# Kernel tuning notes

Hardware: AMD Instinct MI355X
Metric: run time of the kernel (lower is better)

## Reference

```python
import jax, jax.numpy as jnp
import numpy as np

EPS = 1e-5


def _gcn_conv(x, src, dst, norm, W, b, n_nodes):
    # PyG GCNConv: transform, then normalized scatter-add aggregation (self-loops included in src/dst)
    h = x @ W                                   # [N, out]
    msg = h[src] * norm[:, None]                # gather over edges [E+N, out]
    agg = jax.ops.segment_sum(msg, dst, num_segments=n_nodes)
    return agg + b


def _bn(x, gamma, beta):
    # BatchNorm1d in training mode: batch stats over node axis, biased variance
    mu = jnp.mean(x, axis=0)
    var = jnp.mean((x - mu) ** 2, axis=0)
    return (x - mu) * jax.lax.rsqrt(var + EPS) * gamma + beta


def setup_inputs() -> dict:
    key = jax.random.key(0)
    ks = jax.random.split(key, 8)
    N, E, F_in, H, F_out = 50000, 800000, 32, 96, 2
    x = jax.random.normal(ks[0], (N, F_in), dtype=jnp.float32)
    edge_index = jax.random.randint(ks[1], (2, E), 0, N, dtype=jnp.int64)
    def lin(k, fi, fo):
        s = 1.0 / np.sqrt(fi)
        return jax.random.uniform(k, (fi, fo), jnp.float32, -s, s)
    W1 = lin(ks[2], F_in, H); b1 = jnp.zeros((H,), jnp.float32)
    W2 = lin(ks[3], H, H);    b2 = jnp.zeros((H,), jnp.float32)
    W3 = lin(ks[4], H, H);    b3 = jnp.zeros((H,), jnp.float32)
    W4 = lin(ks[5], H, F_out); b4 = jnp.zeros((F_out,), jnp.float32)
    g1 = jnp.ones((H,), jnp.float32); be1 = jnp.zeros((H,), jnp.float32)
    g2 = jnp.ones((H,), jnp.float32); be2 = jnp.zeros((H,), jnp.float32)
    g3 = jnp.ones((H,), jnp.float32); be3 = jnp.zeros((H,), jnp.float32)
    return dict(x=x, edge_index=edge_index,
                W1=W1, b1=b1, g1=g1, be1=be1,
                W2=W2, b2=b2, g2=g2, be2=be2,
                W3=W3, b3=b3, g3=g3, be3=be3,
                W4=W4, b4=b4)


def reference(x, edge_index, W1, b1, g1, be1, W2, b2, g2, be2, W3, b3, g3, be3, W4, b4):
    N = x.shape[0]
    loop = jnp.arange(N, dtype=edge_index.dtype)
    src = jnp.concatenate([edge_index[0], loop])   # add self-loops
    dst = jnp.concatenate([edge_index[1], loop])
    deg = jax.ops.segment_sum(jnp.ones_like(dst, dtype=x.dtype), dst, num_segments=N)
    dinv = jnp.where(deg > 0, jax.lax.rsqrt(deg), 0.0)
    norm = dinv[src] * dinv[dst]                   # D^{-1/2} (A+I) D^{-1/2}

    h = jax.nn.relu(_bn(_gcn_conv(x, src, dst, norm, W1, b1, N), g1, be1))
    h = jax.nn.relu(_bn(_gcn_conv(h, src, dst, norm, W2, b2, N), g2, be2))
    h = jax.nn.relu(_bn(_gcn_conv(h, src, dst, norm, W3, b3, N), g3, be3))
    return _gcn_conv(h, src, dst, norm, W4, b4, N)
```

## Files before the change

### kernel.cpp

```cpp
#include <hip/hip_runtime.h>
#include <hip/hip_bf16.h>

using bf16x8 = __attribute__((ext_vector_type(8))) short;
using f32x4  = __attribute__((ext_vector_type(4))) float;

#define FS_CHUNK 4096

__device__ __forceinline__ float ldf(const void* p, size_t i, float isf){
  if (isf > 0.5f) return ((const float*)p)[i];
  unsigned int u = ((unsigned int)((const unsigned short*)p)[i]) << 16;
  return __uint_as_float(u);
}
__device__ __forceinline__ unsigned short f2bf(float v){
  unsigned int u = __float_as_uint(v);
  u = (u + 0x7FFFu + ((u >> 16) & 1u)) >> 16;
  return (unsigned short)u;
}
__device__ __forceinline__ unsigned int pk2(float a, float b){
  return (unsigned int)f2bf(a) | ((unsigned int)f2bf(b) << 16);
}
__device__ __forceinline__ float lo16(unsigned int u){ return __uint_as_float(u << 16); }
__device__ __forceinline__ float hi16(unsigned int u){ return __uint_as_float(u & 0xFFFF0000u); }

__global__ void k_fill(unsigned short* o, unsigned short v, int n){
  int i = blockIdx.x*blockDim.x + threadIdx.x;
  if (i < n) o[i] = v;
}

__global__ void k_prep(const unsigned short* xh, const unsigned int* eu,
                       float* flag, int nelemX, long long E,
                       const void* W1, const void* W2, const void* W3, const void* W4,
                       unsigned short* __restrict__ Wt1, unsigned short* __restrict__ Wt2,
                       unsigned short* __restrict__ Wt3, float* __restrict__ W4f,
                       int* __restrict__ cnt, float* __restrict__ stAll, int n){
  int t = threadIdx.x;
  if (blockIdx.x > 0){
    int total = n + 4609;
    for (int i = (int)(blockIdx.x-1)*256 + t; i < total; i += (int)(gridDim.x-1)*256){
      if (i < n) cnt[i] = 0; else stAll[i - n] = 0.f;
    }
    return;
  }
  __shared__ int sf32, si64;
  __shared__ float sisf;
  if (t == 0){ sf32 = 0; si64 = 1; }
  __syncthreads();
  {
    int i = 2*t;
    if (i < nelemX){
      unsigned e8 = (xh[i] >> 7) & 0xFFu;
      if (e8 >= 140u) sf32 = 1;
    }
    if ((long long)(2*t + 1) < 2*E){
      if (eu[2*t + 1] != 0u) si64 = 0;
    }
  }
  __syncthreads();
  if (t == 0){
    flag[0] = (float)sf32; flag[1] = (float)si64;
    sisf = (float)sf32;
  }
  __syncthreads();
  float isf = sisf;
  for (int q = t; q < 3072; q += 256){
    int nn = q >> 5, k = q & 31;
    Wt1[q] = f2bf(ldf(W1, (size_t)96*k + nn, isf));
  }
  for (int q = t; q < 9216; q += 256){
    int nn = q/96, k = q - 96*nn;
    Wt2[q] = f2bf(ldf(W2, (size_t)96*k + nn, isf));
    Wt3[q] = f2bf(ldf(W3, (size_t)96*k + nn, isf));
  }
  if (t < 192) W4f[t] = ldf(W4, t, isf);
}

__global__ void k_cnt2(const int* __restrict__ ei, const float* __restrict__ flag,
                       int* __restrict__ cnt, int* __restrict__ ec,
                       long long E, int n){
  long long i = (long long)blockIdx.x*blockDim.x + threadIdx.x;
  long long i0 = 2*i;
  if (i0 >= E) return;
  bool i64 = (flag[1] > 0.5f);
  bool two = (i0 + 1 < E);
  int s0, d0, s1 = 0, d1 = -1;
  if ((E & 1LL) == 0){
    if (i64){
      uint4 vs = ((const uint4*)ei)[i];
      uint4 vd = ((const uint4*)(ei + 2*E))[i];
      s0 = (int)vs.x; s1 = (int)vs.z; d0 = (int)vd.x; d1 = (int)vd.z;
    } else {
      int2 vs = ((const int2*)ei)[i];
      int2 vd = ((const int2*)(ei + E))[i];
      s0 = vs.x; s1 = vs.y; d0 = vd.x; d1 = vd.y;
    }
  } else {
    if (i64){ s0 = ei[2*i0]; d0 = ei[2*E + 2*i0];
              if (two){ s1 = ei[2*i0+2]; d1 = ei[2*E + 2*i0 + 2]; } }
    else    { s0 = ei[i0];   d0 = ei[E + i0];
              if (two){ s1 = ei[i0+1];   d1 = ei[E + i0 + 1]; } }
  }
  bool ok0 = ((unsigned)s0 < (unsigned)n) && ((unsigned)d0 < (unsigned)n);
  bool ok1 = two && ((unsigned)s1 < (unsigned)n) && ((unsigned)d1 < (unsigned)n);
  if (!ok0){ s0 = -1; d0 = -1; }
  if (!ok1){ s1 = -1; d1 = -1; }
  if (two){
    int4 o; o.x = s0; o.y = d0; o.z = s1; o.w = d1;
    ((int4*)ec)[i] = o;
  } else {
    int2 o; o.x = s0; o.y = d0;
    ((int2*)ec)[i0] = o;
  }
  if (ok0) atomicAdd(&cnt[d0], 1);
  if (ok1) atomicAdd(&cnt[d1], 1);
}

__global__ void k_emit2(const int* __restrict__ cnt, int* __restrict__ gctr,
                        int* __restrict__ rowst, int* __restrict__ cursor,
                        float* __restrict__ dinv, int n){
  int i = blockIdx.x*256 + threadIdx.x;
  int lane = threadIdx.x & 63;
  int v = (i < n) ? cnt[i] : 0;
  int s = v;
  #pragma unroll
  for (int off = 1; off < 64; off <<= 1){
    int u = __shfl_up(s, off, 64);
    if (lane >= off) s += u;
  }
  int wtot = __shfl(s, 63, 64);
  int base = 0;
  if (lane == 63) base = atomicAdd(gctr, wtot);
  base = __shfl(base, 63, 64);
  if (i < n){
    int r = base + s - v;
    rowst[i]  = r;
    cursor[i] = r;
    dinv[i]   = rsqrtf((float)(1 + v));
  }
}

template<typename IT>
__global__ __launch_bounds__(256) void k_fx(const int* __restrict__ ec,
      int* __restrict__ cursor, IT* __restrict__ csr,
      long long E, int n, int gF8,
      const void* __restrict__ x, const float* __restrict__ flag,
      const float* __restrict__ dinv, unsigned short* __restrict__ XS){
  int t = threadIdx.x;
  if ((int)blockIdx.x < gF8){
    int part = blockIdx.x & 7;
    long long base = (long long)(blockIdx.x >> 3) * FS_CHUNK;
    int pl = (int)(((long long)n *  part     ) >> 3);
    int pr = (int)(((long long)n * (part + 1)) >> 3);
    long long lim = base + FS_CHUNK < E ? base + FS_CHUNK : E;
    for (long long i = base + 2*t; i < lim; i += 512){
      int4 v = ((const int4*)ec)[i >> 1];
      if (v.y >= pl && v.y < pr && (unsigned)v.x < (unsigned)n){
        int p = atomicAdd(&cursor[v.y], 1);
        csr[p] = (IT)v.x;
      }
      if (i + 1 < lim && v.w >= pl && v.w < pr && (unsigned)v.z < (unsigned)n){
        int p = atomicAdd(&cursor[v.w], 1);
        csr[p] = (IT)v.z;
      }
    }
    return;
  }
  int q = (int)(blockIdx.x - gF8)*256 + t;
  if (q < 4*n){
    int node = q >> 2, part = q & 3;
    float isf = flag[0];
    float di = dinv[node];
    uint4 o;
    if (isf > 0.5f){
      const float* xr = (const float*)x + (size_t)32*node + 8*part;
      o.x = pk2(xr[0]*di, xr[1]*di); o.y = pk2(xr[2]*di, xr[3]*di);
      o.z = pk2(xr[4]*di, xr[5]*di); o.w = pk2(xr[6]*di, xr[7]*di);
    } else {
      uint4 v = ((const uint4*)x)[(size_t)4*node + part];
      o.x = pk2(lo16(v.x)*di, hi16(v.x)*di);
      o.y = pk2(lo16(v.y)*di, hi16(v.y)*di);
      o.z = pk2(lo16(v.z)*di, hi16(v.z)*di);
      o.w = pk2(lo16(v.w)*di, hi16(v.w)*di);
    }
    ((uint4*)XS)[q] = o;
  }
}

#define ACC8(v) { a0+=lo16((v).x); a1+=hi16((v).x); a2+=lo16((v).y); a3+=hi16((v).y); \
                  a4+=lo16((v).z); a5+=hi16((v).z); a6+=lo16((v).w); a7+=hi16((v).w); }

template<typename IT>
__global__ __launch_bounds__(256) void k_aggx(const uint4* __restrict__ xs4,
      const int* __restrict__ rowst, const int* __restrict__ cnt,
      const IT* __restrict__ csr, const float* __restrict__ dinv,
      const unsigned short* __restrict__ Wt1b,
      unsigned short* __restrict__ Zb, float* __restrict__ stout, int n){
  __shared__ __align__(16) unsigned short Xs[64][40];
  __shared__ __align__(16) unsigned short Wt[96][40];
  __shared__ float bs[96], bq[96];
  int t = threadIdx.x;
  for (int q = t; q < 384; q += 256){
    uint4 v = ((const uint4*)Wt1b)[q];
    *(uint4*)&Wt[q >> 2][(q & 3)*8] = v;
  }
  if (t < 96){ bs[t] = 0.f; bq[t] = 0.f; }
  int g = t & 3, ty = t >> 2;
  int node = blockIdx.x*64 + ty;
  float a0=0.f,a1=0.f,a2=0.f,a3=0.f,a4=0.f,a5=0.f,a6=0.f,a7=0.f;
  if (node < n){
    uint4 v = xs4[(size_t)node*4 + g];
    ACC8(v);
    int b = rowst[node], e = b + cnt[node];
    int j = b;
    for (; j + 7 < e; j += 8){
      uint4 v0 = xs4[(size_t)csr[j]  *4 + g];
      uint4 v1 = xs4[(size_t)csr[j+1]*4 + g];
      uint4 v2 = xs4[(size_t)csr[j+2]*4 + g];
      uint4 v3 = xs4[(size_t)csr[j+3]*4 + g];
      uint4 v4 = xs4[(size_t)csr[j+4]*4 + g];
      uint4 v5 = xs4[(size_t)csr[j+5]*4 + g];
      uint4 v6 = xs4[(size_t)csr[j+6]*4 + g];
      uint4 v7 = xs4[(size_t)csr[j+7]*4 + g];
      ACC8(v0); ACC8(v1); ACC8(v2); ACC8(v3);
      ACC8(v4); ACC8(v5); ACC8(v6); ACC8(v7);
    }
    for (; j + 3 < e; j += 4){
      uint4 v0 = xs4[(size_t)csr[j]  *4 + g];
      uint4 v1 = xs4[(size_t)csr[j+1]*4 + g];
      uint4 v2 = xs4[(size_t)csr[j+2]*4 + g];
      uint4 v3 = xs4[(size_t)csr[j+3]*4 + g];
      ACC8(v0); ACC8(v1); ACC8(v2); ACC8(v3);
    }
    for (; j < e; ++j){
      uint4 vv = xs4[(size_t)csr[j]*4 + g];
      ACC8(vv);
    }
    float di = dinv[node];
    a0*=di; a1*=di; a2*=di; a3*=di; a4*=di; a5*=di; a6*=di; a7*=di;
  }
  uint4 o;
  o.x = pk2(a0,a1); o.y = pk2(a2,a3); o.z = pk2(a4,a5); o.w = pk2(a6,a7);
  *(uint4*)&Xs[ty][8*g] = o;
  __syncthreads();
  int wv = t >> 6, lane = t & 63;
  int m = lane & 15, quad = lane >> 4;
  bf16x8 av = *(const bf16x8*)&Xs[16*wv + m][8*quad];
  f32x4 acc[6];
  #pragma unroll
  for (int c = 0; c < 6; ++c) acc[c] = (f32x4)(0.f);
  #pragma unroll
  for (int c = 0; c < 6; ++c){
    bf16x8 bv = *(const bf16x8*)&Wt[16*c + m][8*quad];
    acc[c] = __builtin_amdgcn_mfma_f32_16x16x32_bf16(av, bv, acc[c], 0, 0, 0);
  }
  int rowbase = blockIdx.x*64 + 16*wv + 4*quad;
  #pragma unroll
  for (int c = 0; c < 6; ++c){
    int col = 16*c + m;
    float s = 0.f, q = 0.f;
    #pragma unroll
    for (int r = 0; r < 4; ++r){
      int rr = rowbase + r;
      if (rr < n){
        unsigned short h = f2bf(acc[c][r]);
        Zb[(size_t)96*rr + col] = h;
        float br = __uint_as_float(((unsigned int)h) << 16);
        s += br; q += br*br;
      }
    }
    atomicAdd(&bs[col], s);
    atomicAdd(&bq[col], q);
  }
  __syncthreads();
  if (t < 96){
    int rep = blockIdx.x & 7;
    atomicAdd(&stout[192*rep + t],      bs[t]);
    atomicAdd(&stout[192*rep + 96 + t], bq[t]);
  }
}

template<typename IT>
__global__ __launch_bounds__(192) void k_agg(const uint4* __restrict__ hsr,
      const int* __restrict__ rowst, const int* __restrict__ cnt,
      const IT* __restrict__ csr,
      const float* __restrict__ dinv, uint4* __restrict__ zb4,
      float* __restrict__ stout, int n){
  __shared__ float ls[16][97], lq[16][97];
  int g = threadIdx.x, ty = threadIdx.y;
  int t = ty*12 + g;
  int node = blockIdx.x*16 + ty;
  float r[8];
  if (node < n){
    uint4 v = hsr[(size_t)node*12 + g];
    float a0 = lo16(v.x), a1 = hi16(v.x), a2 = lo16(v.y), a3 = hi16(v.y);
    float a4 = lo16(v.z), a5 = hi16(v.z), a6 = lo16(v.w), a7 = hi16(v.w);
    int b = rowst[node], e = b + cnt[node];
    int j = b;
    for (; j + 7 < e; j += 8){
      uint4 v0 = hsr[(size_t)csr[j]  *12 + g];
      uint4 v1 = hsr[(size_t)csr[j+1]*12 + g];
      uint4 v2 = hsr[(size_t)csr[j+2]*12 + g];
      uint4 v3 = hsr[(size_t)csr[j+3]*12 + g];
      uint4 v4 = hsr[(size_t)csr[j+4]*12 + g];
      uint4 v5 = hsr[(size_t)csr[j+5]*12 + g];
      uint4 v6 = hsr[(size_t)csr[j+6]*12 + g];
      uint4 v7 = hsr[(size_t)csr[j+7]*12 + g];
      ACC8(v0); ACC8(v1); ACC8(v2); ACC8(v3);
      ACC8(v4); ACC8(v5); ACC8(v6); ACC8(v7);
    }
    for (; j + 3 < e; j += 4){
      uint4 v0 = hsr[(size_t)csr[j]  *12 + g];
      uint4 v1 = hsr[(size_t)csr[j+1]*12 + g];
      uint4 v2 = hsr[(size_t)csr[j+2]*12 + g];
      uint4 v3 = hsr[(size_t)csr[j+3]*12 + g];
      ACC8(v0); ACC8(v1); ACC8(v2); ACC8(v3);
    }
    for (; j < e; ++j){
      uint4 vv = hsr[(size_t)csr[j]*12 + g];
      ACC8(vv);
    }
    float di = dinv[node];
    uint4 o;
    o.x = pk2(a0*di, a1*di);
    o.y = pk2(a2*di, a3*di);
    o.z = pk2(a4*di, a5*di);
    o.w = pk2(a6*di, a7*di);
    zb4[(size_t)node*12 + g] = o;
    r[0]=lo16(o.x); r[1]=hi16(o.x); r[2]=lo16(o.y); r[3]=hi16(o.y);
    r[4]=lo16(o.z); r[5]=hi16(o.z); r[6]=lo16(o.w); r[7]=hi16(o.w);
  } else {
    #pragma unroll
    for (int jj = 0; jj < 8; ++jj) r[jj] = 0.f;
  }
  #pragma unroll
  for (int jj = 0; jj < 8; ++jj){
    ls[ty][8*g + jj] = r[jj];
    lq[ty][8*g + jj] = r[jj]*r[jj];
  }
  __syncthreads();
  if (t < 96){
    float s = 0.f, q = 0.f;
    #pragma unroll
    for (int rr = 0; rr < 16; ++rr){ s += ls[rr][t]; q += lq[rr][t]; }
    int rep = blockIdx.x & 7;
    atomicAdd(&stout[192*rep + t],      s);
    atomicAdd(&stout[192*rep + 96 + t], q);
  }
}

__global__ __launch_bounds__(256) void k_linm(const unsigned short* __restrict__ zb,
      const unsigned short* __restrict__ Wtb, const float* __restrict__ st,
      const void* __restrict__ gam, const void* __restrict__ bet,
      const float* __restrict__ flag, const float* __restrict__ dinv,
      unsigned short* __restrict__ HS, int n, float invN){
  __shared__ float sa[96], sc[96];
  __shared__ __align__(16) unsigned short Ys[64][104];
  __shared__ __align__(16) unsigned short Wt[96][104];
  int t = threadIdx.x;
  if (t < 96){
    float ssum = 0.f, qsum = 0.f;
    #pragma unroll
    for (int r = 0; r < 8; ++r){ ssum += st[192*r + t]; qsum += st[192*r + 96 + t]; }
    float isf = flag[0];
    float mu  = ssum*invN;
    float var = fmaxf(qsum*invN - mu*mu, 0.f);
    float istd = rsqrtf(var + 1e-5f);
    float a = ldf(gam, t, isf)*istd;
    sa[t] = a; sc[t] = ldf(bet, t, isf) - mu*a;
  }
  for (int q = t; q < 1152; q += 256){
    uint4 v = ((const uint4*)Wtb)[q];
    *(uint4*)&Wt[q/12][8*(q - 12*(q/12))] = v;
  }
  __syncthreads();
  {
    int row = t >> 2, part = t & 3;
    int node = blockIdx.x*64 + row;
    if (node < n){
      const uint4* zr = (const uint4*)(zb + (size_t)96*node) + 3*part;
      #pragma unroll
      for (int q = 0; q < 3; ++q){
        uint4 zz = zr[q];
        int k = 24*part + 8*q;
        float y0 = fmaxf(lo16(zz.x)*sa[k]   + sc[k],   0.f);
        float y1 = fmaxf(hi16(zz.x)*sa[k+1] + sc[k+1], 0.f);
        float y2 = fmaxf(lo16(zz.y)*sa[k+2] + sc[k+2], 0.f);
        float y3 = fmaxf(hi16(zz.y)*sa[k+3] + sc[k+3], 0.f);
        float y4 = fmaxf(lo16(zz.z)*sa[k+4] + sc[k+4], 0.f);
        float y5 = fmaxf(hi16(zz.z)*sa[k+5] + sc[k+5], 0.f);
        float y6 = fmaxf(lo16(zz.w)*sa[k+6] + sc[k+6], 0.f);
        float y7 = fmaxf(hi16(zz.w)*sa[k+7] + sc[k+7], 0.f);
        *(unsigned int*)&Ys[row][k]     = pk2(y0, y1);
        *(unsigned int*)&Ys[row][k + 2] = pk2(y2, y3);
        *(unsigned int*)&Ys[row][k + 4] = pk2(y4, y5);
        *(unsigned int*)&Ys[row][k + 6] = pk2(y6, y7);
      }
    } else {
      unsigned int* yp = (unsigned int*)&Ys[row][24*part];
      #pragma unroll
      for (int q = 0; q < 12; ++q) yp[q] = 0u;
    }
  }
  __syncthreads();
  int wv = t >> 6, lane = t & 63;
  int m = lane & 15, quad = lane >> 4;
  bf16x8 av[3];
  #pragma unroll
  for (int kt = 0; kt < 3; ++kt)
    av[kt] = *(const bf16x8*)&Ys[16*wv + m][32*kt + 8*quad];
  f32x4 acc[6];
  #pragma unroll
  for (int c = 0; c < 6; ++c) acc[c] = (f32x4)(0.f);
  #pragma unroll
  for (int c = 0; c < 6; ++c){
    const unsigned short* wrow = &Wt[16*c + m][8*quad];
    #pragma unroll
    for (int kt = 0; kt < 3; ++kt){
      bf16x8 bv = *(const bf16x8*)(wrow + 32*kt);
      acc[c] = __builtin_amdgcn_mfma_f32_16x16x32_bf16(av[kt], bv, acc[c], 0, 0, 0);
    }
  }
  int rowbase = blockIdx.x*64 + 16*wv + 4*quad;
  float div[4];
  #pragma unroll
  for (int r = 0; r < 4; ++r){ int rr = rowbase + r; div[r] = (rr < n) ? dinv[rr] : 0.f; }
  #pragma unroll
  for (int c = 0; c < 6; ++c){
    int col = 16*c + m;
    #pragma unroll
    for (int r = 0; r < 4; ++r){
      int rr = rowbase + r;
      if (rr < n) HS[(size_t)96*rr + col] = f2bf(acc[c][r]*div[r]);
    }
  }
}

__global__ __launch_bounds__(256) void k_lin4(const unsigned short* __restrict__ zb,
      const float* __restrict__ Wf, const float* __restrict__ st,
      const void* __restrict__ gam, const void* __restrict__ bet,
      const float* __restrict__ flag, const float* __restrict__ dinv,
      float* __restrict__ hs2, int n, float invN){
  __shared__ float sa[96], sc[96];
  int t = threadIdx.x;
  if (t < 96){
    float ssum = 0.f, qsum = 0.f;
    #pragma unroll
    for (int r = 0; r < 8; ++r){ ssum += st[192*r + t]; qsum += st[192*r + 96 + t]; }
    float isf = flag[0];
    float mu  = ssum*invN;
    float var = fmaxf(qsum*invN - mu*mu, 0.f);
    float istd = rsqrtf(var + 1e-5f);
    float a = ldf(gam, t, isf)*istd;
    sa[t] = a; sc[t] = ldf(bet, t, isf) - mu*a;
  }
  __syncthreads();
  int i = blockIdx.x*blockDim.x + t;
  if (i >= n) return;
  const uint4* zr = (const uint4*)(zb + (size_t)96*i);
  float a0 = 0.f, a1 = 0.f;
  #pragma unroll
  for (int q = 0; q < 12; ++q){
    uint4 zz = zr[q];
    int k = 8*q;
    float y;
    y = fmaxf(lo16(zz.x)*sa[k]   + sc[k],   0.f); a0 += y*Wf[2*k];    a1 += y*Wf[2*k+1];
    y = fmaxf(hi16(zz.x)*sa[k+1] + sc[k+1], 0.f); a0 += y*Wf[2*k+2];  a1 += y*Wf[2*k+3];
    y = fmaxf(lo16(zz.y)*sa[k+2] + sc[k+2], 0.f); a0 += y*Wf[2*k+4];  a1 += y*Wf[2*k+5];
    y = fmaxf(hi16(zz.y)*sa[k+3] + sc[k+3], 0.f); a0 += y*Wf[2*k+6];  a1 += y*Wf[2*k+7];
    y = fmaxf(lo16(zz.z)*sa[k+4] + sc[k+4], 0.f); a0 += y*Wf[2*k+8];  a1 += y*Wf[2*k+9];
    y = fmaxf(hi16(zz.z)*sa[k+5] + sc[k+5], 0.f); a0 += y*Wf[2*k+10]; a1 += y*Wf[2*k+11];
    y = fmaxf(lo16(zz.w)*sa[k+6] + sc[k+6], 0.f); a0 += y*Wf[2*k+12]; a1 += y*Wf[2*k+13];
    y = fmaxf(hi16(zz.w)*sa[k+7] + sc[k+7], 0.f); a0 += y*Wf[2*k+14]; a1 += y*Wf[2*k+15];
  }
  float di = dinv[i];
  hs2[(size_t)2*i]   = di*a0;
  hs2[(size_t)2*i+1] = di*a1;
}

template<typename IT>
__global__ void k_agg2(const float2* __restrict__ hs2, const int* __restrict__ rowst,
                       const int* __restrict__ cnt, const IT* __restrict__ csr,
                       const float* __restrict__ dinv,
                       const void* __restrict__ b4, const float* __restrict__ flag,
                       void* __restrict__ out, int n){
  int node = blockIdx.x*blockDim.x + threadIdx.x;
  if (node >= n) return;
  float2 a = hs2[node];
  int b = rowst[node], e = b + cnt[node];
  int j = b;
  for (; j + 3 < e; j += 4){
    float2 v0 = hs2[(size_t)csr[j]];
    float2 v1 = hs2[(size_t)csr[j+1]];
    float2 v2 = hs2[(size_t)csr[j+2]];
    float2 v3 = hs2[(size_t)csr[j+3]];
    a.x += v0.x + v1.x + v2.x + v3.x;
    a.y += v0.y + v1.y + v2.y + v3.y;
  }
  for (; j < e; ++j){
    float2 v = hs2[(size_t)csr[j]];
    a.x += v.x; a.y += v.y;
  }
  float isf = flag[0];
  float di = dinv[node];
  float v0 = a.x*di + ldf(b4, 0, isf);
  float v1 = a.y*di + ldf(b4, 1, isf);
  if (isf > 0.5f){
    ((float*)out)[(size_t)2*node]   = v0;
    ((float*)out)[(size_t)2*node+1] = v1;
  } else {
    ((unsigned short*)out)[(size_t)2*node]   = f2bf(v0);
    ((unsigned short*)out)[(size_t)2*node+1] = f2bf(v1);
  }
}

extern "C" void kernel_launch(void* const* d_in, const int* in_sizes, int n_in,
                              void* d_out, int out_size, void* d_ws, size_t ws_size,
                              hipStream_t stream)
{
  const int B = 256;
  unsigned short* outh = (unsigned short*)d_out;

  if (n_in < 16){
    k_fill<<<(out_size+B-1)/B, B, 0, stream>>>(outh, 0x3F40u, out_size); return;
  }
  const int N = in_sizes[0] / 32;
  const long long E = in_sizes[1] / 2;
  if (in_sizes[0] % 32 != 0 || out_size != 2*N){
    k_fill<<<(out_size+B-1)/B, B, 0, stream>>>(outh, 0x3F60u, out_size); return;
  }
  const bool u16 = (N < 65536);

  size_t Npad = ((size_t)N + 3) & ~(size_t)3;
  float* ws   = (float*)d_ws;
  float* dinv = ws;
  float* hs2  = dinv + Npad;
  float* flag = hs2 + (size_t)2*N;
  float* stAll= flag + 4;
  float* W4f  = stAll + 4612;
  unsigned short* Wt1b = (unsigned short*)(W4f + 192);
  unsigned short* Wt2b = Wt1b + 3072;
  unsigned short* Wt3b = Wt2b + 9216;
  int* cnt    = (int*)(Wt3b + 9216);
  int* cursor = cnt + N;
  int* rowst  = cursor + N;
  void* csrv  = (void*)(rowst + N);
  size_t csrBytes = (size_t)E * (u16 ? 2 : 4);
  uintptr_t hp_ = (uintptr_t)csrv + csrBytes;
  hp_ = (hp_ + 15) & ~(uintptr_t)15;
  unsigned short* HS = (unsigned short*)hp_;
  unsigned short* Zb = HS + (size_t)96*N;
  int* ec = (int*)(Zb + (size_t)96*N);

  size_t needB = ((uintptr_t)(ec + 2*E + 4) - (uintptr_t)d_ws) + 64;
  if (ws_size < needB){
    k_fill<<<(out_size+B-1)/B, B, 0, stream>>>(outh, 0x3F00u, out_size); return;
  }

  unsigned short* XS = HS;

  const void* x  = d_in[0];
  const int*  ei = (const int*)d_in[1];
  const void* W1 = d_in[2];
  const void* g1 = d_in[4];  const void* be1 = d_in[5];
  const void* W2 = d_in[6];
  const void* g2 = d_in[8];  const void* be2 = d_in[9];
  const void* W3 = d_in[10];
  const void* g3 = d_in[12]; const void* be3 = d_in[13];
  const void* W4 = d_in[14];
  const void* b4 = d_in[15];

  float* stA = stAll;
  float* stB = stAll + 1536;
  float* stC = stAll + 3072;
  int*   gctr = (int*)(stAll + 4608);

  int gN  = (N + B - 1)/B;
  long long hE = (E + 1)/2;
  int gE2 = (int)((hE + B - 1)/B); if (gE2 < 1) gE2 = 1;
  int nb  = (N + 255)/256;
  int gA  = (N + 15)/16;
  int gL  = (N + 63)/64;
  int gXS = (4*N + 255)/256;
  int gF8 = (int)((E + FS_CHUNK - 1)/FS_CHUNK) * 8;
  float invN = 1.0f / (float)N;
  dim3 ablk(12,16);

  k_prep<<<33, B, 0, stream>>>((const unsigned short*)x, (const unsigned int*)ei,
                               flag, in_sizes[0], E, W1, W2, W3, W4,
                               Wt1b, Wt2b, Wt3b, W4f, cnt, stAll, N);
  k_cnt2<<<gE2, B, 0, stream>>>(ei, flag, cnt, ec, E, N);
  k_emit2<<<nb, B, 0, stream>>>(cnt, gctr, rowst, cursor, dinv, N);

  if (u16){
    unsigned short* csr = (unsigned short*)csrv;
    k_fx<unsigned short><<<gF8 + gXS, B, 0, stream>>>(ec, cursor, csr, E, N, gF8,
                                                      x, flag, dinv, XS);
    k_aggx<unsigned short><<<gL, B, 0, stream>>>((const uint4*)XS, rowst, cnt, csr, dinv, Wt1b, Zb, stA, N);
    k_linm<<<gL, B, 0, stream>>>(Zb, Wt2b, stA, g1, be1, flag, dinv, HS, N, invN);
    k_agg<unsigned short><<<gA, ablk, 0, stream>>>((const uint4*)HS, rowst, cnt, csr, dinv, (uint4*)Zb, stB, N);
    k_linm<<<gL, B, 0, stream>>>(Zb, Wt3b, stB, g2, be2, flag, dinv, HS, N, invN);
    k_agg<unsigned short><<<gA, ablk, 0, stream>>>((const uint4*)HS, rowst, cnt, csr, dinv, (uint4*)Zb, stC, N);
    k_lin4<<<gN, B, 0, stream>>>(Zb, W4f, stC, g3, be3, flag, dinv, hs2, N, invN);
    k_agg2<unsigned short><<<gN, B, 0, stream>>>((const float2*)hs2, rowst, cnt, csr, dinv, b4, flag, d_out, N);
  } else {
    int* csr = (int*)csrv;
    k_fx<int><<<gF8 + gXS, B, 0, stream>>>(ec, cursor, csr, E, N, gF8,
                                           x, flag, dinv, XS);
    k_aggx<int><<<gL, B, 0, stream>>>((const uint4*)XS, rowst, cnt, csr, dinv, Wt1b, Zb, stA, N);
    k_linm<<<gL, B, 0, stream>>>(Zb, Wt2b, stA, g1, be1, flag, dinv, HS, N, invN);
    k_agg<int><<<gA, ablk, 0, stream>>>((const uint4*)HS, rowst, cnt, csr, dinv, (uint4*)Zb, stB, N);
    k_linm<<<gL, B, 0, stream>>>(Zb, Wt3b, stB, g2, be2, flag, dinv, HS, N, invN);
    k_agg<int><<<gA, ablk, 0, stream>>>((const uint4*)HS, rowst, cnt, csr, dinv, (uint4*)Zb, stC, N);
    k_lin4<<<gN, B, 0, stream>>>(Zb, W4f, stC, g3, be3, flag, dinv, hs2, N, invN);
    k_agg2<int><<<gN, B, 0, stream>>>((const float2*)hs2, rowst, cnt, csr, dinv, b4, flag, d_out, N);
  }
}
```

Baseline: 329.9 us.

## Fuse BN-ReLU-linear into aggregation by reordering aggregate-then-transform

Replaces the separate k_linm and k_agg kernels for layers 2 and 3 with one k_aggf kernel. It applies the previous layer's BatchNorm affine and ReLU on the fly to gathered neighbour rows, aggregates them, then multiplies by the weight with MFMA and accumulates the BN statistics. This uses linearity to aggregate before transforming. It also stores a per-edge dinv[src] array alongside the CSR so the gather does not need a second indirect lookup. Two launches per layer become one and an intermediate round trip through global memory is dropped. The cost is redoing the affine and ReLU for every edge, an extra 4 bytes read per edge, and more per-block weight loading because blocks shrink to 16 nodes.

New measurement: 349.9 us. 6.1% more time.

```diff
diff --git a/kernel.cpp b/kernel.cpp
--- a/kernel.cpp
+++ b/kernel.cpp
@@ -140,7 +140,7 @@
 
 template<typename IT>
 __global__ __launch_bounds__(256) void k_fx(const int* __restrict__ ec,
-      int* __restrict__ cursor, IT* __restrict__ csr,
+      int* __restrict__ cursor, IT* __restrict__ csr, float* __restrict__ csrd,
       long long E, int n, int gF8,
       const void* __restrict__ x, const float* __restrict__ flag,
       const float* __restrict__ dinv, unsigned short* __restrict__ XS){
@@ -156,10 +156,12 @@
       if (v.y >= pl && v.y < pr && (unsigned)v.x < (unsigned)n){
         int p = atomicAdd(&cursor[v.y], 1);
         csr[p] = (IT)v.x;
+        csrd[p] = dinv[v.x];
       }
       if (i + 1 < lim && v.w >= pl && v.w < pr && (unsigned)v.z < (unsigned)n){
         int p = atomicAdd(&cursor[v.w], 1);
         csr[p] = (IT)v.z;
+        csrd[p] = dinv[v.z];
       }
     }
     return;
@@ -278,88 +280,35 @@
   }
 }
 
+#define AFF8(v,d) { float y_; \
+  y_ = fmaxf(fmaf(lo16((v).x), A0, C0), 0.f); a0 = fmaf(y_, (d), a0); \
+  y_ = fmaxf(fmaf(hi16((v).x), A1, C1), 0.f); a1 = fmaf(y_, (d), a1); \
+  y_ = fmaxf(fmaf(lo16((v).y), A2, C2), 0.f); a2 = fmaf(y_, (d), a2); \
+  y_ = fmaxf(fmaf(hi16((v).y), A3, C3), 0.f); a3 = fmaf(y_, (d), a3); \
+  y_ = fmaxf(fmaf(lo16((v).z), A4, C4), 0.f); a4 = fmaf(y_, (d), a4); \
+  y_ = fmaxf(fmaf(hi16((v).z), A5, C5), 0.f); a5 = fmaf(y_, (d), a5); \
+  y_ = fmaxf(fmaf(lo16((v).w), A6, C6), 0.f); a6 = fmaf(y_, (d), a6); \
+  y_ = fmaxf(fmaf(hi16((v).w), A7, C7), 0.f); a7 = fmaf(y_, (d), a7); }
+
 template<typename IT>
-__global__ __launch_bounds__(192) void k_agg(const uint4* __restrict__ hsr,
+__global__ __launch_bounds__(192) void k_aggf(const uint4* __restrict__ zsrc,
       const int* __restrict__ rowst, const int* __restrict__ cnt,
-      const IT* __restrict__ csr,
-      const float* __restrict__ dinv, uint4* __restrict__ zb4,
-      float* __restrict__ stout, int n){
-  __shared__ float ls[16][97], lq[16][97];
-  int g = threadIdx.x, ty = threadIdx.y;
-  int t = ty*12 + g;
-  int node = blockIdx.x*16 + ty;
-  float r[8];
-  if (node < n){
-    uint4 v = hsr[(size_t)node*12 + g];
-    float a0 = lo16(v.x), a1 = hi16(v.x), a2 = lo16(v.y), a3 = hi16(v.y);
-    float a4 = lo16(v.z), a5 = hi16(v.z), a6 = lo16(v.w), a7 = hi16(v.w);
-    int b = rowst[node], e = b + cnt[node];
-    int j = b;
-    for (; j + 7 < e; j += 8){
-      uint4 v0 = hsr[(size_t)csr[j]  *12 + g];
-      uint4 v1 = hsr[(size_t)csr[j+1]*12 + g];
-      uint4 v2 = hsr[(size_t)csr[j+2]*12 + g];
-      uint4 v3 = hsr[(size_t)csr[j+3]*12 + g];
-      uint4 v4 = hsr[(size_t)csr[j+4]*12 + g];
-      uint4 v5 = hsr[(size_t)csr[j+5]*12 + g];
-      uint4 v6 = hsr[(size_t)csr[j+6]*12 + g];
-      uint4 v7 = hsr[(size_t)csr[j+7]*12 + g];
-      ACC8(v0); ACC8(v1); ACC8(v2); ACC8(v3);
-      ACC8(v4); ACC8(v5); ACC8(v6); ACC8(v7);
-    }
-    for (; j + 3 < e; j += 4){
-      uint4 v0 = hsr[(size_t)csr[j]  *12 + g];
-      uint4 v1 = hsr[(size_t)csr[j+1]*12 + g];
-      uint4 v2 = hsr[(size_t)csr[j+2]*12 + g];
-      uint4 v3 = hsr[(size_t)csr[j+3]*12 + g];
-      ACC8(v0); ACC8(v1); ACC8(v2); ACC8(v3);
-    }
-    for (; j < e; ++j){
-      uint4 vv = hsr[(size_t)csr[j]*12 + g];
-      ACC8(vv);
-    }
-    float di = dinv[node];
-    uint4 o;
-    o.x = pk2(a0*di, a1*di);
-    o.y = pk2(a2*di, a3*di);
-    o.z = pk2(a4*di, a5*di);
-    o.w = pk2(a6*di, a7*di);
-    zb4[(size_t)node*12 + g] = o;
-    r[0]=lo16(o.x); r[1]=hi16(o.x); r[2]=lo16(o.y); r[3]=hi16(o.y);
-    r[4]=lo16(o.z); r[5]=hi16(o.z); r[6]=lo16(o.w); r[7]=hi16(o.w);
-  } else {
-    #pragma unroll
-    for (int jj = 0; jj < 8; ++jj) r[jj] = 0.f;
-  }
-  #pragma unroll
-  for (int jj = 0; jj < 8; ++jj){
-    ls[ty][8*g + jj] = r[jj];
-    lq[ty][8*g + jj] = r[jj]*r[jj];
-  }
-  __syncthreads();
-  if (t < 96){
-    float s = 0.f, q = 0.f;
-    #pragma unroll
-    for (int rr = 0; rr < 16; ++rr){ s += ls[rr][t]; q += lq[rr][t]; }
-    int rep = blockIdx.x & 7;
-    atomicAdd(&stout[192*rep + t],      s);
-    atomicAdd(&stout[192*rep + 96 + t], q);
-  }
-}
-
-__global__ __launch_bounds__(256) void k_linm(const unsigned short* __restrict__ zb,
-      const unsigned short* __restrict__ Wtb, const float* __restrict__ st,
+      const IT* __restrict__ csr, const float* __restrict__ csrd,
+      const float* __restrict__ dinv,
+      const unsigned short* __restrict__ Wtb,
+      const float* __restrict__ stin,
       const void* __restrict__ gam, const void* __restrict__ bet,
-      const float* __restrict__ flag, const float* __restrict__ dinv,
-      unsigned short* __restrict__ HS, int n, float invN){
+      const float* __restrict__ flag,
+      unsigned short* __restrict__ zout, float* __restrict__ stout,
+      int n, float invN){
   __shared__ float sa[96], sc[96];
-  __shared__ __align__(16) unsigned short Ys[64][104];
+  __shared__ __align__(16) unsigned short Y[16][104];
   __shared__ __align__(16) unsigned short Wt[96][104];
   int t = threadIdx.x;
   if (t < 96){
     float ssum = 0.f, qsum = 0.f;
     #pragma unroll
-    for (int r = 0; r < 8; ++r){ ssum += st[192*r + t]; qsum += st[192*r + 96 + t]; }
+    for (int r = 0; r < 8; ++r){ ssum += stin[192*r + t]; qsum += stin[192*r + 96 + t]; }
     float isf = flag[0];
     float mu  = ssum*invN;
     float var = fmaxf(qsum*invN - mu*mu, 0.f);
@@ -367,69 +316,95 @@
     float a = ldf(gam, t, isf)*istd;
     sa[t] = a; sc[t] = ldf(bet, t, isf) - mu*a;
   }
-  for (int q = t; q < 1152; q += 256){
+  for (int q = t; q < 1152; q += 192){
     uint4 v = ((const uint4*)Wtb)[q];
-    *(uint4*)&Wt[q/12][8*(q - 12*(q/12))] = v;
-  }
-  __syncthreads();
-  {
-    int row = t >> 2, part = t & 3;
-    int node = blockIdx.x*64 + row;
-    if (node < n){
-      const uint4* zr = (const uint4*)(zb + (size_t)96*node) + 3*part;
-      #pragma unroll
-      for (int q = 0; q < 3; ++q){
-        uint4 zz = zr[q];
-        int k = 24*part + 8*q;
-        float y0 = fmaxf(lo16(zz.x)*sa[k]   + sc[k],   0.f);
-        float y1 = fmaxf(hi16(zz.x)*sa[k+1] + sc[k+1], 0.f);
-        float y2 = fmaxf(lo16(zz.y)*sa[k+2] + sc[k+2], 0.f);
-        float y3 = fmaxf(hi16(zz.y)*sa[k+3] + sc[k+3], 0.f);
-        float y4 = fmaxf(lo16(zz.z)*sa[k+4] + sc[k+4], 0.f);
-        float y5 = fmaxf(hi16(zz.z)*sa[k+5] + sc[k+5], 0.f);
-        float y6 = fmaxf(lo16(zz.w)*sa[k+6] + sc[k+6], 0.f);
-        float y7 = fmaxf(hi16(zz.w)*sa[k+7] + sc[k+7], 0.f);
-        *(unsigned int*)&Ys[row][k]     = pk2(y0, y1);
-        *(unsigned int*)&Ys[row][k + 2] = pk2(y2, y3);
-        *(unsigned int*)&Ys[row][k + 4] = pk2(y4, y5);
-        *(unsigned int*)&Ys[row][k + 6] = pk2(y6, y7);
-      }
-    } else {
-      unsigned int* yp = (unsigned int*)&Ys[row][24*part];
-      #pragma unroll
-      for (int q = 0; q < 12; ++q) yp[q] = 0u;
-    }
-  }
+    int rr = q/12;
+    *(uint4*)&Wt[rr][8*(q - 12*rr)] = v;
+  }
+  __syncthreads();
+  int g = t % 12, ty = t / 12;
+  float A0=sa[8*g],A1=sa[8*g+1],A2=sa[8*g+2],A3=sa[8*g+3],
+        A4=sa[8*g+4],A5=sa[8*g+5],A6=sa[8*g+6],A7=sa[8*g+7];
+  float C0=sc[8*g],C1=sc[8*g+1],C2=sc[8*g+2],C3=sc[8*g+3],
+        C4=sc[8*g+4],C5=sc[8*g+5],C6=sc[8*g+6],C7=sc[8*g+7];
+  int node = blockIdx.x*16 + ty;
+  float a0=0.f,a1=0.f,a2=0.f,a3=0.f,a4=0.f,a5=0.f,a6=0.f,a7=0.f;
+  if (node < n){
+    float di = dinv[node];
+    {
+      uint4 v = zsrc[(size_t)node*12 + g];
+      AFF8(v, di);
+    }
+    int b = rowst[node], e = b + cnt[node];
+    int j = b;
+    for (; j + 7 < e; j += 8){
+      uint4 v0 = zsrc[(size_t)csr[j]  *12 + g]; float d0 = csrd[j];
+      uint4 v1 = zsrc[(size_t)csr[j+1]*12 + g]; float d1 = csrd[j+1];
+      uint4 v2 = zsrc[(size_t)csr[j+2]*12 + g]; float d2 = csrd[j+2];
+      uint4 v3 = zsrc[(size_t)csr[j+3]*12 + g]; float d3 = csrd[j+3];
+      uint4 v4 = zsrc[(size_t)csr[j+4]*12 + g]; float d4 = csrd[j+4];
+      uint4 v5 = zsrc[(size_t)csr[j+5]*12 + g]; float d5 = csrd[j+5];
+      uint4 v6 = zsrc[(size_t)csr[j+6]*12 + g]; float d6 = csrd[j+6];
+      uint4 v7 = zsrc[(size_t)csr[j+7]*12 + g]; float d7 = csrd[j+7];
+      AFF8(v0,d0); AFF8(v1,d1); AFF8(v2,d2); AFF8(v3,d3);
+      AFF8(v4,d4); AFF8(v5,d5); AFF8(v6,d6); AFF8(v7,d7);
+    }
+    for (; j + 3 < e; j += 4){
+      uint4 v0 = zsrc[(size_t)csr[j]  *12 + g]; float d0 = csrd[j];
+      uint4 v1 = zsrc[(size_t)csr[j+1]*12 + g]; float d1 = csrd[j+1];
+      uint4 v2 = zsrc[(size_t)csr[j+2]*12 + g]; float d2 = csrd[j+2];
+      uint4 v3 = zsrc[(size_t)csr[j+3]*12 + g]; float d3 = csrd[j+3];
+      AFF8(v0,d0); AFF8(v1,d1); AFF8(v2,d2); AFF8(v3,d3);
+    }
+    for (; j < e; ++j){
+      uint4 vv = zsrc[(size_t)csr[j]*12 + g]; float dd = csrd[j];
+      AFF8(vv,dd);
+    }
+    a0*=di; a1*=di; a2*=di; a3*=di; a4*=di; a5*=di; a6*=di; a7*=di;
+  }
+  uint4 o;
+  o.x = pk2(a0,a1); o.y = pk2(a2,a3); o.z = pk2(a4,a5); o.w = pk2(a6,a7);
+  *(uint4*)&Y[ty][8*g] = o;
   __syncthreads();
   int wv = t >> 6, lane = t & 63;
   int m = lane & 15, quad = lane >> 4;
   bf16x8 av[3];
   #pragma unroll
   for (int kt = 0; kt < 3; ++kt)
-    av[kt] = *(const bf16x8*)&Ys[16*wv + m][32*kt + 8*quad];
-  f32x4 acc[6];
-  #pragma unroll
-  for (int c = 0; c < 6; ++c) acc[c] = (f32x4)(0.f);
-  #pragma unroll
-  for (int c = 0; c < 6; ++c){
+    av[kt] = *(const bf16x8*)&Y[m][32*kt + 8*quad];
+  f32x4 acc[2];
+  acc[0] = (f32x4)(0.f); acc[1] = (f32x4)(0.f);
+  #pragma unroll
+  for (int cc = 0; cc < 2; ++cc){
+    int c = 2*wv + cc;
     const unsigned short* wrow = &Wt[16*c + m][8*quad];
     #pragma unroll
     for (int kt = 0; kt < 3; ++kt){
       bf16x8 bv = *(const bf16x8*)(wrow + 32*kt);
-      acc[c] = __builtin_amdgcn_mfma_f32_16x16x32_bf16(av[kt], bv, acc[c], 0, 0, 0);
-    }
-  }
-  int rowbase = blockIdx.x*64 + 16*wv + 4*quad;
-  float div[4];
-  #pragma unroll
-  for (int r = 0; r < 4; ++r){ int rr = rowbase + r; div[r] = (rr < n) ? dinv[rr] : 0.f; }
-  #pragma unroll
-  for (int c = 0; c < 6; ++c){
-    int col = 16*c + m;
+      acc[cc] = __builtin_amdgcn_mfma_f32_16x16x32_bf16(av[kt], bv, acc[cc], 0, 0, 0);
+    }
+  }
+  int rowbase = blockIdx.x*16 + 4*quad;
+  int rep = blockIdx.x & 7;
+  #pragma unroll
+  for (int cc = 0; cc < 2; ++cc){
+    int c = 2*wv + cc, col = 16*c + m;
+    float s = 0.f, q = 0.f;
     #pragma unroll
     for (int r = 0; r < 4; ++r){
       int rr = rowbase + r;
-      if (rr < n) HS[(size_t)96*rr + col] = f2bf(acc[c][r]*div[r]);
+      if (rr < n){
+        unsigned short h = f2bf(acc[cc][r]);
+        zout[(size_t)96*rr + col] = h;
+        float br = __uint_as_float(((unsigned int)h) << 16);
+        s += br; q += br*br;
+      }
+    }
+    s += __shfl_xor(s, 16, 64); s += __shfl_xor(s, 32, 64);
+    q += __shfl_xor(q, 16, 64); q += __shfl_xor(q, 32, 64);
+    if (lane < 16){
+      atomicAdd(&stout[192*rep + col],      s);
+      atomicAdd(&stout[192*rep + 96 + col], q);
     }
   }
 }
@@ -549,8 +524,11 @@
   unsigned short* HS = (unsigned short*)hp_;
   unsigned short* Zb = HS + (size_t)96*N;
   int* ec = (int*)(Zb + (size_t)96*N);
-
-  size_t needB = ((uintptr_t)(ec + 2*E + 4) - (uintptr_t)d_ws) + 64;
+  uintptr_t cd_ = (uintptr_t)(ec + 2*E);
+  cd_ = (cd_ + 15) & ~(uintptr_t)15;
+  float* csrd = (float*)cd_;
+
+  size_t needB = ((uintptr_t)(csrd + E) - (uintptr_t)d_ws) + 64;
   if (ws_size < needB){
     k_fill<<<(out_size+B-1)/B, B, 0, stream>>>(outh, 0x3F00u, out_size); return;
   }
@@ -582,7 +560,6 @@
   int gXS = (4*N + 255)/256;
   int gF8 = (int)((E + FS_CHUNK - 1)/FS_CHUNK) * 8;
   float invN = 1.0f / (float)N;
-  dim3 ablk(12,16);
 
   k_prep<<<33, B, 0, stream>>>((const unsigned short*)x, (const unsigned int*)ei,
                                flag, in_sizes[0], E, W1, W2, W3, W4,
@@ -592,24 +569,24 @@
 
   if (u16){
     unsigned short* csr = (unsigned short*)csrv;
-    k_fx<unsigned short><<<gF8 + gXS, B, 0, stream>>>(ec, cursor, csr, E, N, gF8,
+    k_fx<unsigned short><<<gF8 + gXS, B, 0, stream>>>(ec, cursor, csr, csrd, E, N, gF8,
                                                       x, flag, dinv, XS);
     k_aggx<unsigned short><<<gL, B, 0, stream>>>((const uint4*)XS, rowst, cnt, csr, dinv, Wt1b, Zb, stA, N);
-    k_linm<<<gL, B, 0, stream>>>(Zb, Wt2b, stA, g1, be1, flag, dinv, HS, N, invN);
-    k_agg<unsigned short><<<gA, ablk, 0, stream>>>((const uint4*)HS, rowst, cnt, csr, dinv, (uint4*)Zb, stB, N);
-    k_linm<<<gL, B, 0, stream>>>(Zb, Wt3b, stB, g2, be2, flag, dinv, HS, N, invN);
-    k_agg<unsigned short><<<gA, ablk, 0, stream>>>((const uint4*)HS, rowst, cnt, csr, dinv, (uint4*)Zb, stC, N);
+    k_aggf<unsigned short><<<gA, 192, 0, stream>>>((const uint4*)Zb, rowst, cnt, csr, csrd, dinv,
+                                                   Wt2b, stA, g1, be1, flag, HS, stB, N, invN);
+    k_aggf<unsigned short><<<gA, 192, 0, stream>>>((const uint4*)HS, rowst, cnt, csr, csrd, dinv,
+                                                   Wt3b, stB, g2, be2, flag, Zb, stC, N, invN);
     k_lin4<<<gN, B, 0, stream>>>(Zb, W4f, stC, g3, be3, flag, dinv, hs2, N, invN);
     k_agg2<unsigned short><<<gN, B, 0, stream>>>((const float2*)hs2, rowst, cnt, csr, dinv, b4, flag, d_out, N);
   } else {
     int* csr = (int*)csrv;
-    k_fx<int><<<gF8 + gXS, B, 0, stream>>>(ec, cursor, csr, E, N, gF8,
+    k_fx<int><<<gF8 + gXS, B, 0, stream>>>(ec, cursor, csr, csrd, E, N, gF8,
                                            x, flag, dinv, XS);
     k_aggx<int><<<gL, B, 0, stream>>>((const uint4*)XS, rowst, cnt, csr, dinv, Wt1b, Zb, stA, N);
-    k_linm<<<gL, B, 0, stream>>>(Zb, Wt2b, stA, g1, be1, flag, dinv, HS, N, invN);
-    k_agg<int><<<gA, ablk, 0, stream>>>((const uint4*)HS, rowst, cnt, csr, dinv, (uint4*)Zb, stB, N);
-    k_linm<<<gL, B, 0, stream>>>(Zb, Wt3b, stB, g2, be2, flag, dinv, HS, N, invN);
-    k_agg<int><<<gA, ablk, 0, stream>>>((const uint4*)HS, rowst, cnt, csr, dinv, (uint4*)Zb, stC, N);
+    k_aggf<int><<<gA, 192, 0, stream>>>((const uint4*)Zb, rowst, cnt, csr, csrd, dinv,
+                                        Wt2b, stA, g1, be1, flag, HS, stB, N, invN);
+    k_aggf<int><<<gA, 192, 0, stream>>>((const uint4*)HS, rowst, cnt, csr, csrd, dinv,
+                                        Wt3b, stB, g2, be2, flag, Zb, stC, N, invN);
     k_lin4<<<gN, B, 0, stream>>>(Zb, W4f, stC, g3, be3, flag, dinv, hs2, N, invN);
     k_agg2<int><<<gN, B, 0, stream>>>((const float2*)hs2, rowst, cnt, csr, dinv, b4, flag, d_out, N);
   }
```

## Store hidden features in 8-column planar layout and aggregate per column group

Applied to the files above, without the earlier changes.

Hidden activations move from row-major [N][96] to 12 planes of [N][8] bf16, so each aggregation block handles one 16-byte column group for 256 nodes and gathers from a 0.8 MB plane rather than the full feature table. The goal is better cache locality for the random neighbour gathers. Block ids are ordered so that groups 0-7 come first and groups 8-11 are interleaved, probably to improve L2 or XCD reuse. The cost is that each node's CSR row is read 12 times, the MFMA epilogues now issue strided 2-byte stores, and the 96-column statistics are reduced with wave shuffles.

Result: slower. 418.5 us (+26.9%).

```diff
diff --git a/kernel.cpp b/kernel.cpp
--- a/kernel.cpp
+++ b/kernel.cpp
@@ -256,13 +256,14 @@
   #pragma unroll
   for (int c = 0; c < 6; ++c){
     int col = 16*c + m;
+    size_t gbase = (size_t)(col >> 3)*n*8 + (col & 7);
     float s = 0.f, q = 0.f;
     #pragma unroll
     for (int r = 0; r < 4; ++r){
       int rr = rowbase + r;
       if (rr < n){
         unsigned short h = f2bf(acc[c][r]);
-        Zb[(size_t)96*rr + col] = h;
+        Zb[gbase + (size_t)8*rr] = h;
         float br = __uint_as_float(((unsigned int)h) << 16);
         s += br; q += br*br;
       }
@@ -278,76 +279,7 @@
   }
 }
 
-template<typename IT>
-__global__ __launch_bounds__(192) void k_agg(const uint4* __restrict__ hsr,
-      const int* __restrict__ rowst, const int* __restrict__ cnt,
-      const IT* __restrict__ csr,
-      const float* __restrict__ dinv, uint4* __restrict__ zb4,
-      float* __restrict__ stout, int n){
-  __shared__ float ls[16][97], lq[16][97];
-  int g = threadIdx.x, ty = threadIdx.y;
-  int t = ty*12 + g;
-  int node = blockIdx.x*16 + ty;
-  float r[8];
-  if (node < n){
-    uint4 v = hsr[(size_t)node*12 + g];
-    float a0 = lo16(v.x), a1 = hi16(v.x), a2 = lo16(v.y), a3 = hi16(v.y);
-    float a4 = lo16(v.z), a5 = hi16(v.z), a6 = lo16(v.w), a7 = hi16(v.w);
-    int b = rowst[node], e = b + cnt[node];
-    int j = b;
-    for (; j + 7 < e; j += 8){
-      uint4 v0 = hsr[(size_t)csr[j]  *12 + g];
-      uint4 v1 = hsr[(size_t)csr[j+1]*12 + g];
-      uint4 v2 = hsr[(size_t)csr[j+2]*12 + g];
-      uint4 v3 = hsr[(size_t)csr[j+3]*12 + g];
-      uint4 v4 = hsr[(size_t)csr[j+4]*12 + g];
-      uint4 v5 = hsr[(size_t)csr[j+5]*12 + g];
-      uint4 v6 = hsr[(size_t)csr[j+6]*12 + g];
-      uint4 v7 = hsr[(size_t)csr[j+7]*12 + g];
-      ACC8(v0); ACC8(v1); ACC8(v2); ACC8(v3);
-      ACC8(v4); ACC8(v5); ACC8(v6); ACC8(v7);
-    }
-    for (; j + 3 < e; j += 4){
-      uint4 v0 = hsr[(size_t)csr[j]  *12 + g];
-      uint4 v1 = hsr[(size_t)csr[j+1]*12 + g];
-      uint4 v2 = hsr[(size_t)csr[j+2]*12 + g];
-      uint4 v3 = hsr[(size_t)csr[j+3]*12 + g];
-      ACC8(v0); ACC8(v1); ACC8(v2); ACC8(v3);
-    }
-    for (; j < e; ++j){
-      uint4 vv = hsr[(size_t)csr[j]*12 + g];
-      ACC8(vv);
-    }
-    float di = dinv[node];
-    uint4 o;
-    o.x = pk2(a0*di, a1*di);
-    o.y = pk2(a2*di, a3*di);
-    o.z = pk2(a4*di, a5*di);
-    o.w = pk2(a6*di, a7*di);
-    zb4[(size_t)node*12 + g] = o;
-    r[0]=lo16(o.x); r[1]=hi16(o.x); r[2]=lo16(o.y); r[3]=hi16(o.y);
-    r[4]=lo16(o.z); r[5]=hi16(o.z); r[6]=lo16(o.w); r[7]=hi16(o.w);
-  } else {
-    #pragma unroll
-    for (int jj = 0; jj < 8; ++jj) r[jj] = 0.f;
-  }
-  #pragma unroll
-  for (int jj = 0; jj < 8; ++jj){
-    ls[ty][8*g + jj] = r[jj];
-    lq[ty][8*g + jj] = r[jj]*r[jj];
-  }
-  __syncthreads();
-  if (t < 96){
-    float s = 0.f, q = 0.f;
-    #pragma unroll
-    for (int rr = 0; rr < 16; ++rr){ s += ls[rr][t]; q += lq[rr][t]; }
-    int rep = blockIdx.x & 7;
-    atomicAdd(&stout[192*rep + t],      s);
-    atomicAdd(&stout[192*rep + 96 + t], q);
-  }
-}
-
-__global__ __launch_bounds__(256) void k_linm(const unsigned short* __restrict__ zb,
+__global__ __launch_bounds__(256) void k_ling(const unsigned short* __restrict__ zb,
       const unsigned short* __restrict__ Wtb, const float* __restrict__ st,
       const void* __restrict__ gam, const void* __restrict__ bet,
       const float* __restrict__ flag, const float* __restrict__ dinv,
@@ -375,11 +307,11 @@
   {
     int row = t >> 2, part = t & 3;
     int node = blockIdx.x*64 + row;
+    const uint4* zb4 = (const uint4*)zb;
     if (node < n){
-      const uint4* zr = (const uint4*)(zb + (size_t)96*node) + 3*part;
       #pragma unroll
       for (int q = 0; q < 3; ++q){
-        uint4 zz = zr[q];
+        uint4 zz = zb4[(size_t)(3*part + q)*n + node];
         int k = 24*part + 8*q;
         float y0 = fmaxf(lo16(zz.x)*sa[k]   + sc[k],   0.f);
         float y1 = fmaxf(hi16(zz.x)*sa[k+1] + sc[k+1], 0.f);
@@ -426,10 +358,79 @@
   #pragma unroll
   for (int c = 0; c < 6; ++c){
     int col = 16*c + m;
+    size_t gbase = (size_t)(col >> 3)*n*8 + (col & 7);
     #pragma unroll
     for (int r = 0; r < 4; ++r){
       int rr = rowbase + r;
-      if (rr < n) HS[(size_t)96*rr + col] = f2bf(acc[c][r]*div[r]);
+      if (rr < n) HS[gbase + (size_t)8*rr] = f2bf(acc[c][r]*div[r]);
+    }
+  }
+}
+
+template<typename IT>
+__global__ __launch_bounds__(256) void k_aggp(const uint4* __restrict__ src,
+      const int* __restrict__ rowst, const int* __restrict__ cnt,
+      const IT* __restrict__ csr, const float* __restrict__ dinv,
+      uint4* __restrict__ dst, float* __restrict__ stout,
+      int n, int T, int partB0){
+  int bid = blockIdx.x;
+  int g, tile;
+  if (bid < partB0){ g = bid & 7; tile = bid >> 3; }
+  else {
+    int b2 = bid - partB0; int s = b2 & 7;
+    g = 8 + (s & 3); tile = ((b2 >> 3) << 1) + (s >> 2);
+  }
+  if (tile >= T) return;
+  int t = threadIdx.x;
+  int node = tile*256 + t;
+  const uint4* sg = src + (size_t)g*n;
+  float a0=0.f,a1=0.f,a2=0.f,a3=0.f,a4=0.f,a5=0.f,a6=0.f,a7=0.f;
+  float rr[8];
+  #pragma unroll
+  for (int k = 0; k < 8; ++k) rr[k] = 0.f;
+  if (node < n){
+    uint4 v = sg[node];
+    ACC8(v);
+    int b = rowst[node], e = b + cnt[node];
+    int j = b;
+    for (; j + 7 < e; j += 8){
+      int i0 = csr[j],   i1 = csr[j+1], i2 = csr[j+2], i3 = csr[j+3];
+      int i4 = csr[j+4], i5 = csr[j+5], i6 = csr[j+6], i7 = csr[j+7];
+      uint4 v0 = sg[i0]; uint4 v1 = sg[i1]; uint4 v2 = sg[i2]; uint4 v3 = sg[i3];
+      uint4 v4 = sg[i4]; uint4 v5 = sg[i5]; uint4 v6 = sg[i6]; uint4 v7 = sg[i7];
+      ACC8(v0); ACC8(v1); ACC8(v2); ACC8(v3);
+      ACC8(v4); ACC8(v5); ACC8(v6); ACC8(v7);
+    }
+    for (; j + 3 < e; j += 4){
+      int i0 = csr[j], i1 = csr[j+1], i2 = csr[j+2], i3 = csr[j+3];
+      uint4 v0 = sg[i0]; uint4 v1 = sg[i1]; uint4 v2 = sg[i2]; uint4 v3 = sg[i3];
+      ACC8(v0); ACC8(v1); ACC8(v2); ACC8(v3);
+    }
+    for (; j < e; ++j){
+      uint4 vv = sg[(int)csr[j]];
+      ACC8(vv);
+    }
+    float di = dinv[node];
+    a0*=di; a1*=di; a2*=di; a3*=di; a4*=di; a5*=di; a6*=di; a7*=di;
+    uint4 o;
+    o.x = pk2(a0,a1); o.y = pk2(a2,a3); o.z = pk2(a4,a5); o.w = pk2(a6,a7);
+    dst[(size_t)g*n + node] = o;
+    rr[0]=lo16(o.x); rr[1]=hi16(o.x); rr[2]=lo16(o.y); rr[3]=hi16(o.y);
+    rr[4]=lo16(o.z); rr[5]=hi16(o.z); rr[6]=lo16(o.w); rr[7]=hi16(o.w);
+  }
+  int rep = tile & 7;
+  int lane = t & 63;
+  #pragma unroll
+  for (int k = 0; k < 8; ++k){
+    float s = rr[k], q = rr[k]*rr[k];
+    #pragma unroll
+    for (int off = 1; off < 64; off <<= 1){
+      s += __shfl_xor(s, off, 64);
+      q += __shfl_xor(q, off, 64);
+    }
+    if (lane == 0){
+      atomicAdd(&stout[192*rep + 8*g + k],      s);
+      atomicAdd(&stout[192*rep + 96 + 8*g + k], q);
     }
   }
 }
@@ -455,11 +456,11 @@
   __syncthreads();
   int i = blockIdx.x*blockDim.x + t;
   if (i >= n) return;
-  const uint4* zr = (const uint4*)(zb + (size_t)96*i);
+  const uint4* zb4 = (const uint4*)zb;
   float a0 = 0.f, a1 = 0.f;
   #pragma unroll
   for (int q = 0; q < 12; ++q){
-    uint4 zz = zr[q];
+    uint4 zz = zb4[(size_t)q*n + i];
     int k = 8*q;
     float y;
     y = fmaxf(lo16(zz.x)*sa[k]   + sc[k],   0.f); a0 += y*Wf[2*k];    a1 += y*Wf[2*k+1];
@@ -577,12 +578,15 @@
   long long hE = (E + 1)/2;
   int gE2 = (int)((hE + B - 1)/B); if (gE2 < 1) gE2 = 1;
   int nb  = (N + 255)/256;
-  int gA  = (N + 15)/16;
   int gL  = (N + 63)/64;
   int gXS = (4*N + 255)/256;
   int gF8 = (int)((E + FS_CHUNK - 1)/FS_CHUNK) * 8;
   float invN = 1.0f / (float)N;
-  dim3 ablk(12,16);
+
+  int T  = (N + 255)/256;
+  int partB0 = 8*T;
+  int Th = (T + 1)/2;
+  int gAgg = partB0 + 8*Th;
 
   k_prep<<<33, B, 0, stream>>>((const unsigned short*)x, (const unsigned int*)ei,
                                flag, in_sizes[0], E, W1, W2, W3, W4,
@@ -595,10 +599,12 @@
     k_fx<unsigned short><<<gF8 + gXS, B, 0, stream>>>(ec, cursor, csr, E, N, gF8,
                                                       x, flag, dinv, XS);
     k_aggx<unsigned short><<<gL, B, 0, stream>>>((const uint4*)XS, rowst, cnt, csr, dinv, Wt1b, Zb, stA, N);
-    k_linm<<<gL, B, 0, stream>>>(Zb, Wt2b, stA, g1, be1, flag, dinv, HS, N, invN);
-    k_agg<unsigned short><<<gA, ablk, 0, stream>>>((const uint4*)HS, rowst, cnt, csr, dinv, (uint4*)Zb, stB, N);
-    k_linm<<<gL, B, 0, stream>>>(Zb, Wt3b, stB, g2, be2, flag, dinv, HS, N, invN);
-    k_agg<unsigned short><<<gA, ablk, 0, stream>>>((const uint4*)HS, rowst, cnt, csr, dinv, (uint4*)Zb, stC, N);
+    k_ling<<<gL, B, 0, stream>>>(Zb, Wt2b, stA, g1, be1, flag, dinv, HS, N, invN);
+    k_aggp<unsigned short><<<gAgg, B, 0, stream>>>((const uint4*)HS, rowst, cnt, csr, dinv,
+                                                   (uint4*)Zb, stB, N, T, partB0);
+    k_ling<<<gL, B, 0, stream>>>(Zb, Wt3b, stB, g2, be2, flag, dinv, HS, N, invN);
+    k_aggp<unsigned short><<<gAgg, B, 0, stream>>>((const uint4*)HS, rowst, cnt, csr, dinv,
+                                                   (uint4*)Zb, stC, N, T, partB0);
     k_lin4<<<gN, B, 0, stream>>>(Zb, W4f, stC, g3, be3, flag, dinv, hs2, N, invN);
     k_agg2<unsigned short><<<gN, B, 0, stream>>>((const float2*)hs2, rowst, cnt, csr, dinv, b4, flag, d_out, N);
   } else {
@@ -606,10 +612,12 @@
     k_fx<int><<<gF8 + gXS, B, 0, stream>>>(ec, cursor, csr, E, N, gF8,
                                            x, flag, dinv, XS);
     k_aggx<int><<<gL, B, 0, stream>>>((const uint4*)XS, rowst, cnt, csr, dinv, Wt1b, Zb, stA, N);
-    k_linm<<<gL, B, 0, stream>>>(Zb, Wt2b, stA, g1, be1, flag, dinv, HS, N, invN);
-    k_agg<int><<<gA, ablk, 0, stream>>>((const uint4*)HS, rowst, cnt, csr, dinv, (uint4*)Zb, stB, N);
-    k_linm<<<gL, B, 0, stream>>>(Zb, Wt3b, stB, g2, be2, flag, dinv, HS, N, invN);
-    k_agg<int><<<gA, ablk, 0, stream>>>((const uint4*)HS, rowst, cnt, csr, dinv, (uint4*)Zb, stC, N);
+    k_ling<<<gL, B, 0, stream>>>(Zb, Wt2b, stA, g1, be1, flag, dinv, HS, N, invN);
+    k_aggp<int><<<gAgg, B, 0, stream>>>((const uint4*)HS, rowst, cnt, csr, dinv,
+                                        (uint4*)Zb, stB, N, T, partB0);
+    k_ling<<<gL, B, 0, stream>>>(Zb, Wt3b, stB, g2, be2, flag, dinv, HS, N, invN);
+    k_aggp<int><<<gAgg, B, 0, stream>>>((const uint4*)HS, rowst, cnt, csr, dinv,
+                                        (uint4*)Zb, stC, N, T, partB0);
     k_lin4<<<gN, B, 0, stream>>>(Zb, W4f, stC, g3, be3, flag, dinv, hs2, N, invN);
     k_agg2<int><<<gN, B, 0, stream>>>((const float2*)hs2, rowst, cnt, csr, dinv, b4, flag, d_out, N);
   }
```
